# Optimization experiments

Hardware: AMD Instinct MI355X
Metric: run time of the kernel (lower is better)

The kernel has to match this reference:

```python
import jax, jax.numpy as jnp
import numpy as np

N = 100000          # num nodes
E_C = 6_400_000     # connection edges
E_D = 400_000       # destination edges
F_IN = 5
H = 8
BN_EPS = 1e-5
L2_EPS = 1e-12


def setup_inputs() -> dict:
    key = jax.random.key(0)
    ks = jax.random.split(key, 16)
    d = {}
    d["x"] = jax.random.normal(ks[0], (N, F_IN), dtype=jnp.float32)
    d["edge_index_connections"] = jax.random.randint(ks[1], (2, E_C), 0, N, dtype=jnp.int64)
    d["edge_index_destinations"] = jax.random.randint(ks[2], (2, E_D), 0, N, dtype=jnp.int64)
    # SAGEConv weights: lin_l (neighbor aggregate), lin_r (root), no bias
    d["W1l"] = jax.random.normal(ks[3], (H, F_IN), jnp.float32) * 0.3
    d["W1r"] = jax.random.normal(ks[4], (H, F_IN), jnp.float32) * 0.3
    d["W2l"] = jax.random.normal(ks[5], (H, H), jnp.float32) * 0.3
    d["W2r"] = jax.random.normal(ks[6], (H, H), jnp.float32) * 0.3
    d["W3l"] = jax.random.normal(ks[7], (H, H), jnp.float32) * 0.3
    d["W3r"] = jax.random.normal(ks[8], (H, H), jnp.float32) * 0.3
    d["W4l"] = jax.random.normal(ks[9], (H, H), jnp.float32) * 0.3
    d["W4r"] = jax.random.normal(ks[10], (H, H), jnp.float32) * 0.3
    # LazyBatchNorm1d affine params (init gamma=1, beta=0)
    for i in range(1, 5):
        d[f"g{i}"] = jnp.ones((H,), jnp.float32)
        d[f"b{i}"] = jnp.zeros((H,), jnp.float32)
    return d


def _sage(x, ei, Wl, Wr):
    # PyG SAGEConv(mean aggr, normalize=True, bias=False):
    # out = lin_l(mean_{j in N(i)} x_j) + lin_r(x_i); then L2 normalize rows.
    src, dst = ei[0], ei[1]
    msgs = x[src]                                            # [E, F] gather
    s = jax.ops.segment_sum(msgs, dst, num_segments=N)       # [N, F]
    cnt = jax.ops.segment_sum(jnp.ones((ei.shape[1],), x.dtype), dst, num_segments=N)
    mean = s / jnp.maximum(cnt, 1.0)[:, None]                # zero for isolated nodes
    out = mean @ Wl.T + x @ Wr.T                             # [N, H]
    nrm = jnp.linalg.norm(out, axis=-1, keepdims=True)
    return out / jnp.maximum(nrm, L2_EPS)


def _bn(x, g, b):
    # BatchNorm1d in training mode: per-feature batch stats (biased variance)
    m = x.mean(axis=0)
    v = x.var(axis=0)
    return (x - m) * jax.lax.rsqrt(v + BN_EPS) * g + b


def reference(x, edge_index_connections, edge_index_destinations,
              W1l, W1r, W2l, W2r, W3l, W3r, W4l, W4r,
              g1, b1, g2, b2, g3, b3, g4, b4):
    eic = edge_index_connections
    eid = edge_index_destinations
    h = _bn(jax.nn.relu(_sage(x, eic, W1l, W1r)), g1, b1)
    # ITERATIONS_BEFORE_DESTINATION = 1 (conv4 + bn2)
    h = _bn(jax.nn.relu(_sage(h, eic, W4l, W4r)), g2, b2)
    # destination pass (conv2 + bn3)
    h = _bn(jax.nn.relu(_sage(h, eid, W2l, W2r)), g3, b3)
    # ITERATIONS_AFTER_DESTINATION = 2 (conv3 + bn4)
    for _ in range(2):
        h = _bn(jax.nn.relu(_sage(h, eic, W3l, W3r)), g4, b4)
    return h
```

## Files before the change

### kernel.cpp

```cpp
#include <hip/hip_runtime.h>
#include <hip/hip_fp16.h>

#define NN 100000
#define EC 6400000
#define ED 400000
#define BN_EPS 1e-5f
#define NSB ((NN + 255) >> 8)
#define NCH 256
#define CSR_CAP 19200
#define CHUNK_OF(E) (((((E) + NCH - 1) / NCH) + 3) & ~3)


__global__ __launch_bounds__(1024)
void pre_hist_prep(const int* __restrict__ eic, const int* __restrict__ eid,
                   int* __restrict__ bhist_c, int* __restrict__ bhist_d,
                   const float* __restrict__ x, const float* __restrict__ W1l,
                   const float* __restrict__ W1r, float* __restrict__ xp,
                   __half* __restrict__ xp16,
                   float* __restrict__ W1lp, float* __restrict__ W1rp) {
    int blk = blockIdx.x;
    if (blk < 2 * NCH) {
        const int* ei = (blk < NCH) ? eic : eid;
        int E = (blk < NCH) ? EC : ED;
        int* bhist = (blk < NCH) ? bhist_c : bhist_d;
        int k = (blk < NCH) ? blk : blk - NCH;
        __shared__ int h[NSB];
        for (int i = threadIdx.x; i < NSB; i += 1024) h[i] = 0;
        __syncthreads();
        int chunk = CHUNK_OF(E);
        int beg = k * chunk, end = min(E, beg + chunk);
        for (int e = beg + threadIdx.x * 4; e < end; e += 1024 * 4) {
            int4 d4 = *(const int4*)&ei[E + e];
            atomicAdd(&h[d4.x >> 8], 1);
            atomicAdd(&h[d4.y >> 8], 1);
            atomicAdd(&h[d4.z >> 8], 1);
            atomicAdd(&h[d4.w >> 8], 1);
        }
        __syncthreads();
        for (int i = threadIdx.x; i < NSB; i += 1024) bhist[i * NCH + k] = h[i];
    } else {
        int pb = blk - 2 * NCH;
        int t = pb * 1024 + threadIdx.x;
        if (t < 64) {
            int f = t >> 3, k = t & 7;
            W1lp[t] = (k < 5) ? W1l[f * 5 + k] : 0.f;
            W1rp[t] = (k < 5) ? W1r[f * 5 + k] : 0.f;
        }
        for (int idx = t; idx < NN * 8; idx += 32 * 1024) {
            int f = idx & 7, i = idx >> 3;
            float v = (f < 5) ? x[i * 5 + f] : 0.f;
            xp[idx] = v;
            xp16[idx] = __float2half(v);
        }
    }
}

__global__ __launch_bounds__(256)
void row_scan2(int* __restrict__ bhist_c, int* __restrict__ total_c,
               int* __restrict__ bhist_d, int* __restrict__ total_d) {
    int blk = blockIdx.x;
    int* row = (blk < NSB) ? (bhist_c + blk * NCH)
                           : (bhist_d + (blk - NSB) * NCH);
    int* total = (blk < NSB) ? total_c : total_d;
    int bb = (blk < NSB) ? blk : blk - NSB;
    __shared__ int wsum[4];
    int lane = threadIdx.x & 63, w = threadIdx.x >> 6;
    int v = row[threadIdx.x];
    int x = v;
    #pragma unroll
    for (int sh = 1; sh < 64; sh <<= 1) { int y = __shfl_up(x, sh); if (lane >= sh) x += y; }
    if (lane == 63) wsum[w] = x;
    __syncthreads();
    int wb = 0;
    #pragma unroll
    for (int j = 0; j < 4; ++j) if (j < w) wb += wsum[j];
    row[threadIdx.x] = wb + x - v;
    if (threadIdx.x == 255) total[bb] = wb + x;
}

__global__ void base2(const int* __restrict__ total_c, int* __restrict__ bbase_c,
                      const int* __restrict__ total_d, int* __restrict__ bbase_d,
                      float* __restrict__ stats) {
    for (int i = threadIdx.x; i < 5 * 256; i += 256) stats[i] = 0.f;
    __shared__ int wsum[4];
    __shared__ int carry;
    int lane = threadIdx.x & 63, w = threadIdx.x >> 6;
    for (int which = 0; which < 2; ++which) {
        const int* gt = which ? total_d : total_c;
        int* bb = which ? bbase_d : bbase_c;
        if (threadIdx.x == 0) carry = 0;
        __syncthreads();
        for (int s = 0; s < NSB; s += 256) {
            int idx = s + threadIdx.x;
            int v = (idx < NSB) ? gt[idx] : 0;
            int x = v;
            #pragma unroll
            for (int sh = 1; sh < 64; sh <<= 1) { int y = __shfl_up(x, sh); if (lane >= sh) x += y; }
            if (lane == 63) wsum[w] = x;
            __syncthreads();
            int wb = 0;
            #pragma unroll
            for (int j = 0; j < 4; ++j) if (j < w) wb += wsum[j];
            int all = wsum[0] + wsum[1] + wsum[2] + wsum[3];
            if (idx < NSB) bb[idx] = carry + wb + x - v;
            __syncthreads();
            if (threadIdx.x == 0) carry += all;
            __syncthreads();
        }
    }
}

__global__ __launch_bounds__(1024)
void scatter2(const int* __restrict__ eic, const int* __restrict__ eid,
              const int* __restrict__ bhist_c, const int* __restrict__ bbase_c,
              unsigned* __restrict__ packed_c,
              const int* __restrict__ bhist_d, const int* __restrict__ bbase_d,
              unsigned* __restrict__ packed_d) {
    int blk = blockIdx.x;
    const int* ei = (blk < NCH) ? eic : eid;
    int E = (blk < NCH) ? EC : ED;
    const int* bhist = (blk < NCH) ? bhist_c : bhist_d;
    const int* bbase = (blk < NCH) ? bbase_c : bbase_d;
    unsigned* packed = (blk < NCH) ? packed_c : packed_d;
    int k = (blk < NCH) ? blk : blk - NCH;
    __shared__ int cur[NSB];
    for (int b = threadIdx.x; b < NSB; b += 1024)
        cur[b] = bbase[b] + bhist[b * NCH + k];
    __syncthreads();
    int chunk = CHUNK_OF(E);
    int beg = k * chunk, end = min(E, beg + chunk);
    for (int e = beg + threadIdx.x * 4; e < end; e += 1024 * 4) {
        int4 s4 = *(const int4*)&ei[e];
        int4 d4 = *(const int4*)&ei[E + e];
        { int p = atomicAdd(&cur[d4.x >> 8], 1); packed[p] = (unsigned)s4.x | ((unsigned)(d4.x & 255) << 17); }
        { int p = atomicAdd(&cur[d4.y >> 8], 1); packed[p] = (unsigned)s4.y | ((unsigned)(d4.y & 255) << 17); }
        { int p = atomicAdd(&cur[d4.z >> 8], 1); packed[p] = (unsigned)s4.z | ((unsigned)(d4.z & 255) << 17); }
        { int p = atomicAdd(&cur[d4.w >> 8], 1); packed[p] = (unsigned)s4.w | ((unsigned)(d4.w & 255) << 17); }
    }
}

__global__ __launch_bounds__(256)
void csr2(const unsigned* __restrict__ packed_c, const int* __restrict__ bbase_c,
          const int* __restrict__ total_c, int* __restrict__ csr_c,
          int* __restrict__ offs_c, int* __restrict__ deg_c, float* __restrict__ inv_c,
          const unsigned* __restrict__ packed_d, const int* __restrict__ bbase_d,
          const int* __restrict__ total_d, int* __restrict__ csr_d,
          int* __restrict__ offs_d, int* __restrict__ deg_d, float* __restrict__ inv_d) {
    int blk = blockIdx.x;
    const unsigned* packed = (blk < NSB) ? packed_c : packed_d;
    const int* bbase = (blk < NSB) ? bbase_c : bbase_d;
    const int* total = (blk < NSB) ? total_c : total_d;
    int* csr  = (blk < NSB) ? csr_c : csr_d;
    int* offs = (blk < NSB) ? offs_c : offs_d;
    int* deg  = (blk < NSB) ? deg_c : deg_d;
    float* inv = (blk < NSB) ? inv_c : inv_d;
    int b = (blk < NSB) ? blk : blk - NSB;

    __shared__ int h[256];
    __shared__ int loff[256];
    __shared__ int ws2[4];
    __shared__ int ebuf[CSR_CAP];
    int ebeg = bbase[b], ecnt = total[b];
    int node0 = b << 8;
    int nn = min(256, NN - node0);
    h[threadIdx.x] = 0;
    __syncthreads();
    for (int e = threadIdx.x; e < ecnt; e += 256)
        atomicAdd(&h[packed[ebeg + e] >> 17], 1);
    __syncthreads();
    {
        int lane = threadIdx.x & 63, w = threadIdx.x >> 6;
        int v = h[threadIdx.x], x = v;
        #pragma unroll
        for (int sh = 1; sh < 64; sh <<= 1) { int y = __shfl_up(x, sh); if (lane >= sh) x += y; }
        if (lane == 63) ws2[w] = x;
        __syncthreads();
        int wb = 0;
        #pragma unroll
        for (int j = 0; j < 4; ++j) if (j < w) wb += ws2[j];
        int excl = wb + x - v;
        loff[threadIdx.x] = excl;
        if (threadIdx.x < nn) {
            int node = node0 + threadIdx.x;
            offs[node] = ebeg + excl;
            deg[node]  = v;
            inv[node]  = 1.0f / (float)(v > 1 ? v : 1);
        }
    }
    __syncthreads();
    if (ecnt <= CSR_CAP) {
        for (int e = threadIdx.x; e < ecnt; e += 256) {
            unsigned u = packed[ebeg + e];
            int p = atomicAdd(&loff[u >> 17], 1);
            ebuf[p] = (int)(u & 0x1FFFF);
        }
        __syncthreads();
        for (int e = threadIdx.x; e < ecnt; e += 256) csr[ebeg + e] = ebuf[e];
    } else {
        for (int e = threadIdx.x; e < ecnt; e += 256) {
            unsigned u = packed[ebeg + e];
            int p = atomicAdd(&loff[u >> 17], 1);
            csr[ebeg + p] = (int)(u & 0x1FFFF);
        }
    }
}

#define ACC8(RV, M) do { \
    float2 q0 = __half22float2(*(const __half2*)&RV.x); \
    float2 q1 = __half22float2(*(const __half2*)&RV.y); \
    float2 q2 = __half22float2(*(const __half2*)&RV.z); \
    float2 q3 = __half22float2(*(const __half2*)&RV.w); \
    a0 = fmaf(q0.x, M, a0); a1 = fmaf(q0.y, M, a1); \
    a2 = fmaf(q1.x, M, a2); a3 = fmaf(q1.y, M, a3); \
    a4 = fmaf(q2.x, M, a4); a5 = fmaf(q2.y, M, a5); \
    a6 = fmaf(q3.x, M, a6); a7 = fmaf(q3.y, M, a7); \
} while (0)

template<bool APPLY_BN>
__global__ __launch_bounds__(256)
void sage_layer8(const float* __restrict__ hin,
                 const __half* __restrict__ hin16,
                 const float* __restrict__ stats_in,
                 const float* __restrict__ gin, const float* __restrict__ bin,
                 const int* __restrict__ offs, const int* __restrict__ deg,
                 const int* __restrict__ csr, const float* __restrict__ inv,
                 const float* __restrict__ Wl, const float* __restrict__ Wr,
                 float* __restrict__ hout, __half* __restrict__ hout16,
                 float* __restrict__ stats_out) {
    __shared__ float bl[16];
    int tid = threadIdx.x;
    if (tid < 16) bl[tid] = 0.f;
    __syncthreads();
    int wave = tid >> 6, lane = tid & 63, g = lane >> 3, f = lane & 7;

    float wls[8], wrs[8];
    float Bl = 0.f, Br = 0.f;
    #pragma unroll
    for (int k = 0; k < 8; ++k) {
        float w_l = Wl[f * 8 + k], w_r = Wr[f * 8 + k];
        float sck = 1.f, shk = 0.f;
        if constexpr (APPLY_BN) {
            float m = stats_in[k * 16] * (1.f / NN);
            float v = stats_in[(8 + k) * 16] * (1.f / NN) - m * m;
            float is = rsqrtf(v + BN_EPS);
            sck = gin[k] * is;
            shk = bin[k] - m * sck;
        }
        wls[k] = sck * w_l;
        wrs[k] = sck * w_r;
        Bl = fmaf(shk, w_l, Bl);
        Br = fmaf(shk, w_r, Br);
    }

    float acc_r = 0.f, acc_r2 = 0.f;
    const int stride = gridDim.x * 32;
    for (int i0 = (blockIdx.x * 4 + wave) * 8; i0 < NN; i0 += stride) {
        int i = i0 + g;
        int ic = min(i, NN - 1);
        bool ok = (i < NN);
        int d = ok ? deg[ic] : 0;
        int o = offs[ic];
        float im = inv[ic];
        const float4* hp = (const float4*)(hin + (size_t)ic * 8);
        float4 h0 = hp[0];
        float4 h1 = hp[1];
        float a0 = 0, a1 = 0, a2 = 0, a3 = 0, a4 = 0, a5 = 0, a6 = 0, a7 = 0;
        for (int b = 0; b < d; b += 32) {
            int e = b + f * 4;
            const int* cp = csr + o + e;
            int c0 = cp[0], c1 = cp[1], c2 = cp[2], c3 = cp[3];
            bool k0 = (e < d), k1 = (e + 1 < d), k2 = (e + 2 < d), k3 = (e + 3 < d);
            unsigned s0 = k0 ? ((unsigned)c0 & 0x1FFFFu) : 0u;
            unsigned s1 = k1 ? ((unsigned)c1 & 0x1FFFFu) : 0u;
            unsigned s2 = k2 ? ((unsigned)c2 & 0x1FFFFu) : 0u;
            unsigned s3 = k3 ? ((unsigned)c3 & 0x1FFFFu) : 0u;
            uint4 r0 = *(const uint4*)(hin16 + (size_t)s0 * 8);
            uint4 r1 = *(const uint4*)(hin16 + (size_t)s1 * 8);
            uint4 r2 = *(const uint4*)(hin16 + (size_t)s2 * 8);
            uint4 r3 = *(const uint4*)(hin16 + (size_t)s3 * 8);
            float m0 = k0 ? 1.f : 0.f;
            float m1 = k1 ? 1.f : 0.f;
            float m2 = k2 ? 1.f : 0.f;
            float m3 = k3 ? 1.f : 0.f;
            ACC8(r0, m0);
            ACC8(r1, m1);
            ACC8(r2, m2);
            ACC8(r3, m3);
        }
        #pragma unroll
        for (int msk = 1; msk < 8; msk <<= 1) {
            a0 += __shfl_xor(a0, msk); a1 += __shfl_xor(a1, msk);
            a2 += __shfl_xor(a2, msk); a3 += __shfl_xor(a3, msk);
            a4 += __shfl_xor(a4, msk); a5 += __shfl_xor(a5, msk);
            a6 += __shfl_xor(a6, msk); a7 += __shfl_xor(a7, msk);
        }
        float dnz = (d > 0) ? 1.f : 0.f;
        float hk[8] = { h0.x, h0.y, h0.z, h0.w, h1.x, h1.y, h1.z, h1.w };
        float ac[8] = { a0, a1, a2, a3, a4, a5, a6, a7 };
        float y = fmaf(dnz, Bl, Br);
        #pragma unroll
        for (int k = 0; k < 8; ++k) {
            y = fmaf(ac[k] * im, wls[k], y);
            y = fmaf(hk[k], wrs[k], y);
        }
        float n2 = y * y;
        n2 += __shfl_xor(n2, 1);
        n2 += __shfl_xor(n2, 2);
        n2 += __shfl_xor(n2, 4);
        float z = y / fmaxf(sqrtf(n2), 1e-12f);
        float r = fmaxf(z, 0.f);
        r = ok ? r : 0.f;
        if (ok) {
            hout[(size_t)i * 8 + f] = r;
            hout16[(size_t)i * 8 + f] = __float2half(r);
        }
        acc_r += r;
        acc_r2 += r * r;
    }
    atomicAdd(&bl[f], acc_r);
    atomicAdd(&bl[8 + f], acc_r2);
    __syncthreads();
    if (tid < 16) atomicAdd(&stats_out[tid * 16], bl[tid]);
}

__global__ void apply_bn_out(const float* __restrict__ hin,
                             const float* __restrict__ stats,
                             const float* __restrict__ g, const float* __restrict__ b,
                             float* __restrict__ out) {
    int t = blockIdx.x * blockDim.x + threadIdx.x;
    if (t >= NN * 8) return;
    int f = t & 7;
    float m = stats[f * 16] * (1.0f / NN);
    float v = stats[(8 + f) * 16] * (1.0f / NN) - m * m;
    float sc = g[f] * rsqrtf(v + BN_EPS);
    float sh = b[f] - m * sc;
    out[t] = fmaf(hin[t], sc, sh);
}


static inline char* bump(char*& p, size_t bytes) {
    char* r = p;
    p += (bytes + 255) & ~(size_t)255;
    return r;
}

extern "C" void kernel_launch(void* const* d_in, const int* in_sizes, int n_in,
                              void* d_out, int out_size, void* d_ws, size_t ws_size,
                              hipStream_t stream) {
    const float* x   = (const float*)d_in[0];
    const int* eic   = (const int*)d_in[1];
    const int* eid   = (const int*)d_in[2];
    const float* W1l = (const float*)d_in[3];
    const float* W1r = (const float*)d_in[4];
    const float* W2l = (const float*)d_in[5];
    const float* W2r = (const float*)d_in[6];
    const float* W3l = (const float*)d_in[7];
    const float* W3r = (const float*)d_in[8];
    const float* W4l = (const float*)d_in[9];
    const float* W4r = (const float*)d_in[10];
    const float* g1 = (const float*)d_in[11];
    const float* b1 = (const float*)d_in[12];
    const float* g2 = (const float*)d_in[13];
    const float* b2 = (const float*)d_in[14];
    const float* g3 = (const float*)d_in[15];
    const float* b3 = (const float*)d_in[16];
    const float* g4 = (const float*)d_in[17];
    const float* b4 = (const float*)d_in[18];
    float* out = (float*)d_out;

    char* p = (char*)d_ws;
    float* stats   = (float*)bump(p, 5 * 256 * 4);
    int*   bhist_c = (int*)  bump(p, (size_t)NSB * NCH * 4);
    int*   bhist_d = (int*)  bump(p, (size_t)NSB * NCH * 4);
    int*   total_c = (int*)  bump(p, NSB * 4);
    int*   bbase_c = (int*)  bump(p, NSB * 4);
    int*   total_d = (int*)  bump(p, NSB * 4);
    int*   bbase_d = (int*)  bump(p, NSB * 4);
    int*   offs_c  = (int*)  bump(p, NN * 4);
    int*   deg_c   = (int*)  bump(p, NN * 4);
    float* inv_c   = (float*)bump(p, NN * 4);
    int*   offs_d  = (int*)  bump(p, NN * 4);
    int*   deg_d   = (int*)  bump(p, NN * 4);
    float* inv_d   = (float*)bump(p, NN * 4);
    int*   csr_c   = (int*)  bump(p, ((size_t)EC + 64) * 4);
    int*   csr_d   = (int*)  bump(p, ((size_t)ED + 64) * 4);
    float* xp32    = (float*)bump(p, (size_t)NN * 8 * 4);
    __half* xp16   = (__half*)bump(p, (size_t)NN * 8 * 2);
    float* W1lp    = (float*)bump(p, 64 * 4);
    float* W1rp    = (float*)bump(p, 64 * 4);
    unsigned* packed_d = (unsigned*)bump(p, (size_t)ED * 4);
    char* pc = p;
    unsigned* packed_c = (unsigned*)bump(p, (size_t)EC * 4);
    char* pr = pc;
    float*  r_a   = (float*) bump(pr, (size_t)NN * 8 * 4);
    float*  r_b   = (float*) bump(pr, (size_t)NN * 8 * 4);
    __half* h16_a = (__half*)bump(pr, (size_t)NN * 8 * 2);
    __half* h16_b = (__half*)bump(pr, (size_t)NN * 8 * 2);
    (void)ws_size; (void)in_sizes; (void)n_in; (void)out_size;

    pre_hist_prep<<<2 * NCH + 32, 1024, 0, stream>>>(
        eic, eid, bhist_c, bhist_d, x, W1l, W1r, xp32, xp16, W1lp, W1rp);
    row_scan2<<<2 * NSB, 256, 0, stream>>>(bhist_c, total_c, bhist_d, total_d);
    base2<<<1, 256, 0, stream>>>(total_c, bbase_c, total_d, bbase_d, stats);
    scatter2<<<2 * NCH, 1024, 0, stream>>>(
        eic, eid, bhist_c, bbase_c, packed_c, bhist_d, bbase_d, packed_d);
    csr2<<<2 * NSB, 256, 0, stream>>>(
        packed_c, bbase_c, total_c, csr_c, offs_c, deg_c, inv_c,
        packed_d, bbase_d, total_d, csr_d, offs_d, deg_d, inv_d);

    const int LB = 2048;
    sage_layer8<false><<<LB, 256, 0, stream>>>(
        xp32, xp16, nullptr, nullptr, nullptr,
        offs_c, deg_c, csr_c, inv_c, W1lp, W1rp, r_a, h16_a, stats + 0);
    sage_layer8<true><<<LB, 256, 0, stream>>>(
        r_a, h16_a, stats + 0, g1, b1,
        offs_c, deg_c, csr_c, inv_c, W4l, W4r, r_b, h16_b, stats + 256);
    sage_layer8<true><<<LB, 256, 0, stream>>>(
        r_b, h16_b, stats + 256, g2, b2,
        offs_d, deg_d, csr_d, inv_d, W2l, W2r, r_a, h16_a, stats + 512);
    sage_layer8<true><<<LB, 256, 0, stream>>>(
        r_a, h16_a, stats + 512, g3, b3,
        offs_c, deg_c, csr_c, inv_c, W3l, W3r, r_b, h16_b, stats + 768);
    sage_layer8<true><<<LB, 256, 0, stream>>>(
        r_b, h16_b, stats + 768, g4, b4,
        offs_c, deg_c, csr_c, inv_c, W3l, W3r, r_a, h16_a, stats + 1024);
    apply_bn_out<<<(NN * 8 + 255) / 256, 256, 0, stream>>>(r_a, stats + 1024, g4, b4, out);
}
```

Baseline: 580.6 us.

## Fuse CSR build phases into one cooperative kernel with grid syncs

Replaces the five separate CSR-construction launches (histogram, row scan, base scan, scatter, per-bucket sort) with a single cooperative kernel of 391 blocks of 1024 threads that separates phases with grid-wide syncs. The histogram layout changes to NB x NB with each block handling one chunk of both edge lists, and the global base scan is done redundantly per block by a block reduction instead of a single-block scan. This is meant to cut launch gaps and the serial single-block scan, but it needs all 391 large blocks resident at once. If the cooperative launch fails it falls back to five regular launches.

```diff
diff --git a/kernel.cpp b/kernel.cpp
--- a/kernel.cpp
+++ b/kernel.cpp
@@ -1,208 +1,283 @@
 #include <hip/hip_runtime.h>
 #include <hip/hip_fp16.h>
+#include <hip/hip_cooperative_groups.h>
+namespace cg = cooperative_groups;
 
 #define NN 100000
 #define EC 6400000
 #define ED 400000
 #define BN_EPS 1e-5f
-#define NSB ((NN + 255) >> 8)
-#define NCH 256
-#define CSR_CAP 19200
-#define CHUNK_OF(E) (((((E) + NCH - 1) / NCH) + 3) & ~3)
-
-
-__global__ __launch_bounds__(1024)
-void pre_hist_prep(const int* __restrict__ eic, const int* __restrict__ eid,
-                   int* __restrict__ bhist_c, int* __restrict__ bhist_d,
-                   const float* __restrict__ x, const float* __restrict__ W1l,
-                   const float* __restrict__ W1r, float* __restrict__ xp,
-                   __half* __restrict__ xp16,
-                   float* __restrict__ W1lp, float* __restrict__ W1rp) {
-    int blk = blockIdx.x;
-    if (blk < 2 * NCH) {
-        const int* ei = (blk < NCH) ? eic : eid;
-        int E = (blk < NCH) ? EC : ED;
-        int* bhist = (blk < NCH) ? bhist_c : bhist_d;
-        int k = (blk < NCH) ? blk : blk - NCH;
-        __shared__ int h[NSB];
-        for (int i = threadIdx.x; i < NSB; i += 1024) h[i] = 0;
-        __syncthreads();
-        int chunk = CHUNK_OF(E);
-        int beg = k * chunk, end = min(E, beg + chunk);
-        for (int e = beg + threadIdx.x * 4; e < end; e += 1024 * 4) {
-            int4 d4 = *(const int4*)&ei[E + e];
-            atomicAdd(&h[d4.x >> 8], 1);
-            atomicAdd(&h[d4.y >> 8], 1);
-            atomicAdd(&h[d4.z >> 8], 1);
-            atomicAdd(&h[d4.w >> 8], 1);
-        }
-        __syncthreads();
-        for (int i = threadIdx.x; i < NSB; i += 1024) bhist[i * NCH + k] = h[i];
-    } else {
-        int pb = blk - 2 * NCH;
-        int t = pb * 1024 + threadIdx.x;
-        if (t < 64) {
-            int f = t >> 3, k = t & 7;
-            W1lp[t] = (k < 5) ? W1l[f * 5 + k] : 0.f;
-            W1rp[t] = (k < 5) ? W1r[f * 5 + k] : 0.f;
-        }
-        for (int idx = t; idx < NN * 8; idx += 32 * 1024) {
-            int f = idx & 7, i = idx >> 3;
-            float v = (f < 5) ? x[i * 5 + f] : 0.f;
-            xp[idx] = v;
-            xp16[idx] = __float2half(v);
-        }
-    }
-}
-
-__global__ __launch_bounds__(256)
-void row_scan2(int* __restrict__ bhist_c, int* __restrict__ total_c,
-               int* __restrict__ bhist_d, int* __restrict__ total_d) {
-    int blk = blockIdx.x;
-    int* row = (blk < NSB) ? (bhist_c + blk * NCH)
-                           : (bhist_d + (blk - NSB) * NCH);
-    int* total = (blk < NSB) ? total_c : total_d;
-    int bb = (blk < NSB) ? blk : blk - NSB;
-    __shared__ int wsum[4];
-    int lane = threadIdx.x & 63, w = threadIdx.x >> 6;
-    int v = row[threadIdx.x];
+#define NB 391
+#define CK_C 16372
+#define CK_D 1024
+#define CSR_CAP 18240
+#define SMEM_I 18816
+
+
+__device__ __forceinline__ int blockReduceSum1024(int v, int* ws) {
+    int tid = threadIdx.x, lane = tid & 63, w = tid >> 6;
+    #pragma unroll
+    for (int sh = 32; sh; sh >>= 1) v += __shfl_xor(v, sh);
+    if (lane == 0) ws[w] = v;
+    __syncthreads();
+    int s = 0;
+    #pragma unroll
+    for (int j = 0; j < 16; ++j) s += ws[j];
+    __syncthreads();
+    return s;
+}
+
+__device__ __forceinline__ int blockExclScan1024(int v, int* ws) {
+    int tid = threadIdx.x, lane = tid & 63, w = tid >> 6;
     int x = v;
     #pragma unroll
     for (int sh = 1; sh < 64; sh <<= 1) { int y = __shfl_up(x, sh); if (lane >= sh) x += y; }
-    if (lane == 63) wsum[w] = x;
+    if (lane == 63) ws[w] = x;
     __syncthreads();
     int wb = 0;
     #pragma unroll
-    for (int j = 0; j < 4; ++j) if (j < w) wb += wsum[j];
-    row[threadIdx.x] = wb + x - v;
-    if (threadIdx.x == 255) total[bb] = wb + x;
-}
-
-__global__ void base2(const int* __restrict__ total_c, int* __restrict__ bbase_c,
-                      const int* __restrict__ total_d, int* __restrict__ bbase_d,
-                      float* __restrict__ stats) {
-    for (int i = threadIdx.x; i < 5 * 256; i += 256) stats[i] = 0.f;
-    __shared__ int wsum[4];
-    __shared__ int carry;
-    int lane = threadIdx.x & 63, w = threadIdx.x >> 6;
-    for (int which = 0; which < 2; ++which) {
-        const int* gt = which ? total_d : total_c;
-        int* bb = which ? bbase_d : bbase_c;
-        if (threadIdx.x == 0) carry = 0;
+    for (int j = 0; j < 16; ++j) if (j < w) wb += ws[j];
+    __syncthreads();
+    return wb + x - v;
+}
+
+__device__ void phase_hist(int k, int* sm,
+    const int* __restrict__ eic, const int* __restrict__ eid,
+    int* __restrict__ bhist_c, int* __restrict__ bhist_d,
+    const float* __restrict__ x, const float* __restrict__ W1l,
+    const float* __restrict__ W1r, float* __restrict__ xp,
+    __half* __restrict__ xp16, float* __restrict__ W1lp,
+    float* __restrict__ W1rp, float* __restrict__ stats)
+{
+    int tid = threadIdx.x;
+    int* hc = sm;
+    int* hd = sm + NB;
+    for (int i = tid; i < 2 * NB; i += 1024) sm[i] = 0;
+    __syncthreads();
+    {
+        int beg = k * CK_C, end = min(EC, beg + CK_C);
+        for (int e = beg + tid * 4; e < end; e += 4096) {
+            int4 d4 = *(const int4*)&eic[EC + e];
+            atomicAdd(&hc[d4.x >> 8], 1);
+            atomicAdd(&hc[d4.y >> 8], 1);
+            atomicAdd(&hc[d4.z >> 8], 1);
+            atomicAdd(&hc[d4.w >> 8], 1);
+        }
+    }
+    {
+        int beg = k * CK_D, end = min(ED, beg + CK_D);
+        for (int e = beg + tid * 4; e < end; e += 4096) {
+            int4 d4 = *(const int4*)&eid[ED + e];
+            atomicAdd(&hd[d4.x >> 8], 1);
+            atomicAdd(&hd[d4.y >> 8], 1);
+            atomicAdd(&hd[d4.z >> 8], 1);
+            atomicAdd(&hd[d4.w >> 8], 1);
+        }
+    }
+    __syncthreads();
+    for (int i = tid; i < NB; i += 1024) {
+        bhist_c[i * NB + k] = hc[i];
+        bhist_d[i * NB + k] = hd[i];
+    }
+    for (int idx = k * 1024 + tid; idx < NN * 8; idx += NB * 1024) {
+        int f = idx & 7, i = idx >> 3;
+        float v = (f < 5) ? x[i * 5 + f] : 0.f;
+        xp[idx] = v;
+        xp16[idx] = __float2half(v);
+    }
+    if (k == 0) {
+        if (tid < 64) {
+            int f = tid >> 3, kk = tid & 7;
+            W1lp[tid] = (kk < 5) ? W1l[f * 5 + kk] : 0.f;
+            W1rp[tid] = (kk < 5) ? W1r[f * 5 + kk] : 0.f;
+        }
+        for (int i = tid; i < 5 * 256; i += 1024) stats[i] = 0.f;
+    }
+}
+
+__device__ void phase_tot(int b, int* sm,
+    const int* __restrict__ bhist_c, const int* __restrict__ bhist_d,
+    int* __restrict__ total_c, int* __restrict__ total_d)
+{
+    int tid = threadIdx.x;
+    int vc = (tid < NB) ? bhist_c[b * NB + tid] : 0;
+    int vd = (tid < NB) ? bhist_d[b * NB + tid] : 0;
+    int tc = blockReduceSum1024(vc, sm);
+    int td = blockReduceSum1024(vd, sm);
+    if (tid == 0) { total_c[b] = tc; total_d[b] = td; }
+}
+
+__device__ void phase_base(int b, int* sm,
+    int* __restrict__ bhist_c, int* __restrict__ bhist_d,
+    const int* __restrict__ total_c, const int* __restrict__ total_d,
+    int* __restrict__ ebeg_c, int* __restrict__ ebeg_d)
+{
+    int tid = threadIdx.x;
+    int mc = (tid < b) ? total_c[tid] : 0;
+    int md = (tid < b) ? total_d[tid] : 0;
+    int base_c = blockReduceSum1024(mc, sm);
+    int base_d = blockReduceSum1024(md, sm);
+    int vc = (tid < NB) ? bhist_c[b * NB + tid] : 0;
+    int ec = blockExclScan1024(vc, sm);
+    if (tid < NB) bhist_c[b * NB + tid] = base_c + ec;
+    int vd = (tid < NB) ? bhist_d[b * NB + tid] : 0;
+    int ed = blockExclScan1024(vd, sm);
+    if (tid < NB) bhist_d[b * NB + tid] = base_d + ed;
+    if (tid == 0) { ebeg_c[b] = base_c; ebeg_d[b] = base_d; }
+}
+
+__device__ void phase_scatter(int k, int* sm,
+    const int* __restrict__ eic, const int* __restrict__ eid,
+    const int* __restrict__ bhist_c, const int* __restrict__ bhist_d,
+    unsigned* __restrict__ packed_c, unsigned* __restrict__ packed_d)
+{
+    int tid = threadIdx.x;
+    for (int bb = tid; bb < NB; bb += 1024) sm[bb] = bhist_c[bb * NB + k];
+    __syncthreads();
+    {
+        int beg = k * CK_C, end = min(EC, beg + CK_C);
+        for (int e = beg + tid * 4; e < end; e += 4096) {
+            int4 s4 = *(const int4*)&eic[e];
+            int4 d4 = *(const int4*)&eic[EC + e];
+            { int p = atomicAdd(&sm[d4.x >> 8], 1); packed_c[p] = (unsigned)s4.x | ((unsigned)(d4.x & 255) << 17); }
+            { int p = atomicAdd(&sm[d4.y >> 8], 1); packed_c[p] = (unsigned)s4.y | ((unsigned)(d4.y & 255) << 17); }
+            { int p = atomicAdd(&sm[d4.z >> 8], 1); packed_c[p] = (unsigned)s4.z | ((unsigned)(d4.z & 255) << 17); }
+            { int p = atomicAdd(&sm[d4.w >> 8], 1); packed_c[p] = (unsigned)s4.w | ((unsigned)(d4.w & 255) << 17); }
+        }
+    }
+    __syncthreads();
+    for (int bb = tid; bb < NB; bb += 1024) sm[bb] = bhist_d[bb * NB + k];
+    __syncthreads();
+    {
+        int beg = k * CK_D, end = min(ED, beg + CK_D);
+        for (int e = beg + tid * 4; e < end; e += 4096) {
+            int4 s4 = *(const int4*)&eid[e];
+            int4 d4 = *(const int4*)&eid[ED + e];
+            { int p = atomicAdd(&sm[d4.x >> 8], 1); packed_d[p] = (unsigned)s4.x | ((unsigned)(d4.x & 255) << 17); }
+            { int p = atomicAdd(&sm[d4.y >> 8], 1); packed_d[p] = (unsigned)s4.y | ((unsigned)(d4.y & 255) << 17); }
+            { int p = atomicAdd(&sm[d4.z >> 8], 1); packed_d[p] = (unsigned)s4.z | ((unsigned)(d4.z & 255) << 17); }
+            { int p = atomicAdd(&sm[d4.w >> 8], 1); packed_d[p] = (unsigned)s4.w | ((unsigned)(d4.w & 255) << 17); }
+        }
+    }
+    __syncthreads();
+}
+
+__device__ void csr_one(int b, int* sm,
+    const unsigned* __restrict__ packed, const int* __restrict__ ebeg_a,
+    const int* __restrict__ total_a, int* __restrict__ csr,
+    int* __restrict__ offs, int* __restrict__ deg, float* __restrict__ inv)
+{
+    int tid = threadIdx.x;
+    int* h    = sm;
+    int* loff = sm + 256;
+    int* ws   = sm + 512;
+    int* ebuf = sm + 544;
+    int ebeg = ebeg_a[b], ecnt = total_a[b];
+    int node0 = b << 8;
+    int nn = min(256, NN - node0);
+    if (tid < 256) h[tid] = 0;
+    __syncthreads();
+    for (int e = tid; e < ecnt; e += 1024)
+        atomicAdd(&h[packed[ebeg + e] >> 17], 1);
+    __syncthreads();
+    int v = (tid < 256) ? h[tid] : 0;
+    {
+        int lane = tid & 63, w = tid >> 6;
+        int xx = v;
+        #pragma unroll
+        for (int sh = 1; sh < 64; sh <<= 1) { int y = __shfl_up(xx, sh); if (lane >= sh) xx += y; }
+        if (lane == 63 && w < 4) ws[w] = xx;
         __syncthreads();
-        for (int s = 0; s < NSB; s += 256) {
-            int idx = s + threadIdx.x;
-            int v = (idx < NSB) ? gt[idx] : 0;
-            int x = v;
-            #pragma unroll
-            for (int sh = 1; sh < 64; sh <<= 1) { int y = __shfl_up(x, sh); if (lane >= sh) x += y; }
-            if (lane == 63) wsum[w] = x;
-            __syncthreads();
+        if (tid < 256) {
             int wb = 0;
             #pragma unroll
-            for (int j = 0; j < 4; ++j) if (j < w) wb += wsum[j];
-            int all = wsum[0] + wsum[1] + wsum[2] + wsum[3];
-            if (idx < NSB) bb[idx] = carry + wb + x - v;
-            __syncthreads();
-            if (threadIdx.x == 0) carry += all;
-            __syncthreads();
-        }
-    }
-}
-
-__global__ __launch_bounds__(1024)
-void scatter2(const int* __restrict__ eic, const int* __restrict__ eid,
-              const int* __restrict__ bhist_c, const int* __restrict__ bbase_c,
-              unsigned* __restrict__ packed_c,
-              const int* __restrict__ bhist_d, const int* __restrict__ bbase_d,
-              unsigned* __restrict__ packed_d) {
-    int blk = blockIdx.x;
-    const int* ei = (blk < NCH) ? eic : eid;
-    int E = (blk < NCH) ? EC : ED;
-    const int* bhist = (blk < NCH) ? bhist_c : bhist_d;
-    const int* bbase = (blk < NCH) ? bbase_c : bbase_d;
-    unsigned* packed = (blk < NCH) ? packed_c : packed_d;
-    int k = (blk < NCH) ? blk : blk - NCH;
-    __shared__ int cur[NSB];
-    for (int b = threadIdx.x; b < NSB; b += 1024)
-        cur[b] = bbase[b] + bhist[b * NCH + k];
-    __syncthreads();
-    int chunk = CHUNK_OF(E);
-    int beg = k * chunk, end = min(E, beg + chunk);
-    for (int e = beg + threadIdx.x * 4; e < end; e += 1024 * 4) {
-        int4 s4 = *(const int4*)&ei[e];
-        int4 d4 = *(const int4*)&ei[E + e];
-        { int p = atomicAdd(&cur[d4.x >> 8], 1); packed[p] = (unsigned)s4.x | ((unsigned)(d4.x & 255) << 17); }
-        { int p = atomicAdd(&cur[d4.y >> 8], 1); packed[p] = (unsigned)s4.y | ((unsigned)(d4.y & 255) << 17); }
-        { int p = atomicAdd(&cur[d4.z >> 8], 1); packed[p] = (unsigned)s4.z | ((unsigned)(d4.z & 255) << 17); }
-        { int p = atomicAdd(&cur[d4.w >> 8], 1); packed[p] = (unsigned)s4.w | ((unsigned)(d4.w & 255) << 17); }
-    }
-}
-
-__global__ __launch_bounds__(256)
-void csr2(const unsigned* __restrict__ packed_c, const int* __restrict__ bbase_c,
-          const int* __restrict__ total_c, int* __restrict__ csr_c,
-          int* __restrict__ offs_c, int* __restrict__ deg_c, float* __restrict__ inv_c,
-          const unsigned* __restrict__ packed_d, const int* __restrict__ bbase_d,
-          const int* __restrict__ total_d, int* __restrict__ csr_d,
-          int* __restrict__ offs_d, int* __restrict__ deg_d, float* __restrict__ inv_d) {
-    int blk = blockIdx.x;
-    const unsigned* packed = (blk < NSB) ? packed_c : packed_d;
-    const int* bbase = (blk < NSB) ? bbase_c : bbase_d;
-    const int* total = (blk < NSB) ? total_c : total_d;
-    int* csr  = (blk < NSB) ? csr_c : csr_d;
-    int* offs = (blk < NSB) ? offs_c : offs_d;
-    int* deg  = (blk < NSB) ? deg_c : deg_d;
-    float* inv = (blk < NSB) ? inv_c : inv_d;
-    int b = (blk < NSB) ? blk : blk - NSB;
-
-    __shared__ int h[256];
-    __shared__ int loff[256];
-    __shared__ int ws2[4];
-    __shared__ int ebuf[CSR_CAP];
-    int ebeg = bbase[b], ecnt = total[b];
-    int node0 = b << 8;
-    int nn = min(256, NN - node0);
-    h[threadIdx.x] = 0;
-    __syncthreads();
-    for (int e = threadIdx.x; e < ecnt; e += 256)
-        atomicAdd(&h[packed[ebeg + e] >> 17], 1);
-    __syncthreads();
-    {
-        int lane = threadIdx.x & 63, w = threadIdx.x >> 6;
-        int v = h[threadIdx.x], x = v;
-        #pragma unroll
-        for (int sh = 1; sh < 64; sh <<= 1) { int y = __shfl_up(x, sh); if (lane >= sh) x += y; }
-        if (lane == 63) ws2[w] = x;
-        __syncthreads();
-        int wb = 0;
-        #pragma unroll
-        for (int j = 0; j < 4; ++j) if (j < w) wb += ws2[j];
-        int excl = wb + x - v;
-        loff[threadIdx.x] = excl;
-        if (threadIdx.x < nn) {
-            int node = node0 + threadIdx.x;
-            offs[node] = ebeg + excl;
-            deg[node]  = v;
-            inv[node]  = 1.0f / (float)(v > 1 ? v : 1);
+            for (int j = 0; j < 4; ++j) if (j < w) wb += ws[j];
+            int excl = wb + xx - v;
+            loff[tid] = excl;
+            if (tid < nn) {
+                int node = node0 + tid;
+                offs[node] = ebeg + excl;
+                deg[node]  = v;
+                inv[node]  = 1.0f / (float)(v > 1 ? v : 1);
+            }
         }
     }
     __syncthreads();
     if (ecnt <= CSR_CAP) {
-        for (int e = threadIdx.x; e < ecnt; e += 256) {
+        for (int e = tid; e < ecnt; e += 1024) {
             unsigned u = packed[ebeg + e];
             int p = atomicAdd(&loff[u >> 17], 1);
             ebuf[p] = (int)(u & 0x1FFFF);
         }
         __syncthreads();
-        for (int e = threadIdx.x; e < ecnt; e += 256) csr[ebeg + e] = ebuf[e];
+        for (int e = tid; e < ecnt; e += 1024) csr[ebeg + e] = ebuf[e];
     } else {
-        for (int e = threadIdx.x; e < ecnt; e += 256) {
+        for (int e = tid; e < ecnt; e += 1024) {
             unsigned u = packed[ebeg + e];
             int p = atomicAdd(&loff[u >> 17], 1);
             csr[ebeg + p] = (int)(u & 0x1FFFF);
         }
     }
+    __syncthreads();
+}
+
+__global__ __launch_bounds__(1024, 8)
+void coop_prep(const int* eic, const int* eid,
+               int* bhist_c, int* bhist_d,
+               int* total_c, int* total_d, int* ebeg_c, int* ebeg_d,
+               unsigned* packed_c, unsigned* packed_d,
+               int* csr_c, int* offs_c, int* deg_c, float* inv_c,
+               int* csr_d, int* offs_d, int* deg_d, float* inv_d,
+               const float* x, const float* W1l, const float* W1r,
+               float* xp, __half* xp16, float* W1lp, float* W1rp, float* stats)
+{
+    __shared__ int sm[SMEM_I];
+    cg::grid_group g = cg::this_grid();
+    int blk = blockIdx.x;
+    phase_hist(blk, sm, eic, eid, bhist_c, bhist_d, x, W1l, W1r, xp, xp16, W1lp, W1rp, stats);
+    g.sync();
+    phase_tot(blk, sm, bhist_c, bhist_d, total_c, total_d);
+    g.sync();
+    phase_base(blk, sm, bhist_c, bhist_d, total_c, total_d, ebeg_c, ebeg_d);
+    g.sync();
+    phase_scatter(blk, sm, eic, eid, bhist_c, bhist_d, packed_c, packed_d);
+    g.sync();
+    csr_one(blk, sm, packed_c, ebeg_c, total_c, csr_c, offs_c, deg_c, inv_c);
+    csr_one(blk, sm, packed_d, ebeg_d, total_d, csr_d, offs_d, deg_d, inv_d);
+}
+
+__global__ __launch_bounds__(1024, 8)
+void k_hist(const int* eic, const int* eid, int* bhist_c, int* bhist_d,
+            const float* x, const float* W1l, const float* W1r,
+            float* xp, __half* xp16, float* W1lp, float* W1rp, float* stats) {
+    __shared__ int sm[SMEM_I];
+    phase_hist(blockIdx.x, sm, eic, eid, bhist_c, bhist_d, x, W1l, W1r, xp, xp16, W1lp, W1rp, stats);
+}
+__global__ __launch_bounds__(1024, 8)
+void k_tot(const int* bhist_c, const int* bhist_d, int* total_c, int* total_d) {
+    __shared__ int sm[SMEM_I];
+    phase_tot(blockIdx.x, sm, bhist_c, bhist_d, total_c, total_d);
+}
+__global__ __launch_bounds__(1024, 8)
+void k_base(int* bhist_c, int* bhist_d, const int* total_c, const int* total_d,
+            int* ebeg_c, int* ebeg_d) {
+    __shared__ int sm[SMEM_I];
+    phase_base(blockIdx.x, sm, bhist_c, bhist_d, total_c, total_d, ebeg_c, ebeg_d);
+}
+__global__ __launch_bounds__(1024, 8)
+void k_scatter(const int* eic, const int* eid, const int* bhist_c, const int* bhist_d,
+               unsigned* packed_c, unsigned* packed_d) {
+    __shared__ int sm[SMEM_I];
+    phase_scatter(blockIdx.x, sm, eic, eid, bhist_c, bhist_d, packed_c, packed_d);
+}
+__global__ __launch_bounds__(1024, 8)
+void k_csr(const unsigned* packed_c, const int* ebeg_c, const int* total_c,
+           int* csr_c, int* offs_c, int* deg_c, float* inv_c,
+           const unsigned* packed_d, const int* ebeg_d, const int* total_d,
+           int* csr_d, int* offs_d, int* deg_d, float* inv_d) {
+    __shared__ int sm[SMEM_I];
+    csr_one(blockIdx.x, sm, packed_c, ebeg_c, total_c, csr_c, offs_c, deg_c, inv_c);
+    csr_one(blockIdx.x, sm, packed_d, ebeg_d, total_d, csr_d, offs_d, deg_d, inv_d);
 }
 
 #define ACC8(RV, M) do { \
@@ -347,9 +422,9 @@
 extern "C" void kernel_launch(void* const* d_in, const int* in_sizes, int n_in,
                               void* d_out, int out_size, void* d_ws, size_t ws_size,
                               hipStream_t stream) {
-    const float* x   = (const float*)d_in[0];
     const int* eic   = (const int*)d_in[1];
     const int* eid   = (const int*)d_in[2];
+    const float* x   = (const float*)d_in[0];
     const float* W1l = (const float*)d_in[3];
     const float* W1r = (const float*)d_in[4];
     const float* W2l = (const float*)d_in[5];
@@ -370,12 +445,12 @@
 
     char* p = (char*)d_ws;
     float* stats   = (float*)bump(p, 5 * 256 * 4);
-    int*   bhist_c = (int*)  bump(p, (size_t)NSB * NCH * 4);
-    int*   bhist_d = (int*)  bump(p, (size_t)NSB * NCH * 4);
-    int*   total_c = (int*)  bump(p, NSB * 4);
-    int*   bbase_c = (int*)  bump(p, NSB * 4);
-    int*   total_d = (int*)  bump(p, NSB * 4);
-    int*   bbase_d = (int*)  bump(p, NSB * 4);
+    int*   bhist_c = (int*)  bump(p, (size_t)NB * NB * 4);
+    int*   bhist_d = (int*)  bump(p, (size_t)NB * NB * 4);
+    int*   total_c = (int*)  bump(p, NB * 4);
+    int*   total_d = (int*)  bump(p, NB * 4);
+    int*   ebeg_c  = (int*)  bump(p, NB * 4);
+    int*   ebeg_d  = (int*)  bump(p, NB * 4);
     int*   offs_c  = (int*)  bump(p, NN * 4);
     int*   deg_c   = (int*)  bump(p, NN * 4);
     float* inv_c   = (float*)bump(p, NN * 4);
@@ -398,15 +473,26 @@
     __half* h16_b = (__half*)bump(pr, (size_t)NN * 8 * 2);
     (void)ws_size; (void)in_sizes; (void)n_in; (void)out_size;
 
-    pre_hist_prep<<<2 * NCH + 32, 1024, 0, stream>>>(
-        eic, eid, bhist_c, bhist_d, x, W1l, W1r, xp32, xp16, W1lp, W1rp);
-    row_scan2<<<2 * NSB, 256, 0, stream>>>(bhist_c, total_c, bhist_d, total_d);
-    base2<<<1, 256, 0, stream>>>(total_c, bbase_c, total_d, bbase_d, stats);
-    scatter2<<<2 * NCH, 1024, 0, stream>>>(
-        eic, eid, bhist_c, bbase_c, packed_c, bhist_d, bbase_d, packed_d);
-    csr2<<<2 * NSB, 256, 0, stream>>>(
-        packed_c, bbase_c, total_c, csr_c, offs_c, deg_c, inv_c,
-        packed_d, bbase_d, total_d, csr_d, offs_d, deg_d, inv_d);
+    void* cargs[] = {
+        (void*)&eic, (void*)&eid, (void*)&bhist_c, (void*)&bhist_d,
+        (void*)&total_c, (void*)&total_d, (void*)&ebeg_c, (void*)&ebeg_d,
+        (void*)&packed_c, (void*)&packed_d,
+        (void*)&csr_c, (void*)&offs_c, (void*)&deg_c, (void*)&inv_c,
+        (void*)&csr_d, (void*)&offs_d, (void*)&deg_d, (void*)&inv_d,
+        (void*)&x, (void*)&W1l, (void*)&W1r,
+        (void*)&xp32, (void*)&xp16, (void*)&W1lp, (void*)&W1rp, (void*)&stats
+    };
+    hipError_t ce = hipLaunchCooperativeKernel((void*)coop_prep, dim3(NB), dim3(1024),
+                                               cargs, 0, stream);
+    if (ce != hipSuccess) {
+        k_hist<<<NB, 1024, 0, stream>>>(eic, eid, bhist_c, bhist_d,
+                                        x, W1l, W1r, xp32, xp16, W1lp, W1rp, stats);
+        k_tot<<<NB, 1024, 0, stream>>>(bhist_c, bhist_d, total_c, total_d);
+        k_base<<<NB, 1024, 0, stream>>>(bhist_c, bhist_d, total_c, total_d, ebeg_c, ebeg_d);
+        k_scatter<<<NB, 1024, 0, stream>>>(eic, eid, bhist_c, bhist_d, packed_c, packed_d);
+        k_csr<<<NB, 1024, 0, stream>>>(packed_c, ebeg_c, total_c, csr_c, offs_c, deg_c, inv_c,
+                                       packed_d, ebeg_d, total_d, csr_d, offs_d, deg_d, inv_d);
+    }
 
     const int LB = 2048;
     sage_layer8<false><<<LB, 256, 0, stream>>>(
```

After: 782.8 us. +34.8%, slower.
